# Optimization experiments

Measured on AMD Instinct MI355X. Metric: run time of the kernel, lower is better.

Reference implementation:

```python
import jax, jax.numpy as jnp
import numpy as np

L, N, E, H = 2048, 4, 1024, 16
DH = E // H


def setup_inputs() -> dict:
    key = jax.random.key(0)
    k1, k2, k3 = jax.random.split(key, 3)
    x = jax.random.normal(k1, (L, N, E), dtype=jnp.float32)
    # init like nn.Linear-ish scale to keep activations sane
    weight_qkv = jax.random.normal(k2, (3 * E, E), dtype=jnp.float32) * (E ** -0.5)
    weight_out = jax.random.normal(k3, (E, E), dtype=jnp.float32) * (E ** -0.5)
    return {"x": x, "weight_qkv": weight_qkv, "weight_out": weight_out}


def reference(x, weight_qkv, weight_out):
    # x: [L, N, E]; weight_qkv: [3E, E]; weight_out: [E, E]
    l, n, e = x.shape
    # fused QKV projection (F.linear: x @ W^T)
    qkv = jnp.einsum('lne,fe->lnf', x, weight_qkv)          # [L, N, 3E]
    qkv = qkv.reshape(l, n, 3, H, DH)
    q, k, v = jnp.moveaxis(qkv, 2, 0)                       # each [L, N, H, DH]
    q = jnp.transpose(q, (1, 2, 0, 3))                      # [N, H, L, DH]
    k = jnp.transpose(k, (1, 2, 0, 3))
    v = jnp.transpose(v, (1, 2, 0, 3))
    scale = DH ** -0.5
    scores = jnp.einsum('nhld,nhmd->nhlm', q, k) * scale    # [N, H, L, L]
    attn = jax.nn.softmax(scores, axis=-1)                  # dropout p=0.0 -> identity
    ctx = jnp.einsum('nhlm,nhmd->nhld', attn, v)            # [N, H, L, DH]
    ctx = jnp.transpose(ctx, (2, 0, 1, 3)).reshape(l, n, e) # [L, N, E]
    out = jnp.einsum('lne,fe->lnf', ctx, weight_out)        # output projection
    return out
```

## Files before the change

kernel.cpp:

```cpp
#include <hip/hip_runtime.h>
#include <hip/hip_bf16.h>

#define SEQ_L 2048
#define NBATCH 4
#define EDIM 1024
#define NHEAD 16
#define DHEAD 64

typedef __attribute__((ext_vector_type(4))) float f32x4;
typedef __attribute__((ext_vector_type(8))) short short8;
typedef unsigned short u16;
typedef unsigned long long u64;

#define QSCALE (0.125f * 1.44269504088896340736f)

__device__ __forceinline__ u16 f2bf(float f){
  unsigned u = __float_as_uint(f);
  u += 0x7fffu + ((u >> 16) & 1u);
  return (u16)(u >> 16);
}
__device__ __forceinline__ unsigned pack2bf(float a, float b){
  return ((unsigned)f2bf(b) << 16) | (unsigned)f2bf(a);
}
__device__ __forceinline__ u64 pack4bf(float a, float b, float c, float d){
  return ((u64)pack2bf(c, d) << 32) | (u64)pack2bf(a, b);
}
__device__ __forceinline__ float fexp2(float x){
  float r; asm("v_exp_f32 %0, %1" : "=v"(r) : "v"(x)); return r;
}

__global__ __launch_bounds__(256) void cvt_f32_bf16(const float* __restrict__ src,
                                                    u16* __restrict__ dst, int n4){
  int i = blockIdx.x * 256 + threadIdx.x;
  if (i < n4){
    float4 v = reinterpret_cast<const float4*>(src)[i];
    ushort4 o;
    o.x = f2bf(v.x); o.y = f2bf(v.y); o.z = f2bf(v.z); o.w = f2bf(v.w);
    reinterpret_cast<ushort4*>(dst)[i] = o;
  }
}

__global__ __launch_bounds__(256) void qkv_gemm(const u16* __restrict__ X,
                                                const u16* __restrict__ W,
                                                u16* __restrict__ Qd,
                                                u16* __restrict__ Kd,
                                                u16* __restrict__ Vt){
  __shared__ u16 SMEM[2*128*72];
  u16* XL = SMEM;
  u16* WL = SMEM + 128*72;
  const int tid = threadIdx.x;
  const int lane = tid & 63;
  const int wid = tid >> 6;
  const int wr = wid >> 1, wc = wid & 1;
  const int lr = lane & 15, lg = lane >> 4;
  const int bm = blockIdx.x, bn = blockIdx.y;
  f32x4 acc[4][4] = {};
  for (int kt = 0; kt < 16; ++kt){
    __syncthreads();
#pragma unroll
    for (int it = 0; it < 4; ++it){
      int c = tid + 256*it;
      int row = c >> 3, c8 = (c & 7) * 8;
      *(short8*)&XL[row*72 + c8] = *(const short8*)&X[(bm*128 + row)*EDIM + kt*64 + c8];
      *(short8*)&WL[row*72 + c8] = *(const short8*)&W[(bn*128 + row)*EDIM + kt*64 + c8];
    }
    __syncthreads();
#pragma unroll
    for (int ks = 0; ks < 2; ++ks){
      short8 a[4], b[4];
#pragma unroll
      for (int m = 0; m < 4; ++m)  a[m]  = *(short8*)&XL[(wr*64 + m*16  + lr)*72 + ks*32 + lg*8];
#pragma unroll
      for (int nn = 0; nn < 4; ++nn) b[nn] = *(short8*)&WL[(wc*64 + nn*16 + lr)*72 + ks*32 + lg*8];
#pragma unroll
      for (int m = 0; m < 4; ++m)
#pragma unroll
        for (int nn = 0; nn < 4; ++nn)
          acc[m][nn] = __builtin_amdgcn_mfma_f32_16x16x32_bf16(a[m], b[nn], acc[m][nn], 0, 0, 0);
    }
  }
  if (bn < 16){
#pragma unroll
    for (int m = 0; m < 4; ++m){
      const int i0 = bm*128 + wr*64 + m*16 + lg*4;
      const int l = i0 >> 2;
#pragma unroll
      for (int nn = 0; nn < 4; ++nn){
        const int f = bn*128 + wc*64 + nn*16 + lr;
        const int which = f >> 10;
        const int h = (f >> 6) & 15;
        const int d = f & 63;
        u16* dst = (which == 0) ? Qd : Kd;
        const float sc = (which == 0) ? QSCALE : 1.0f;
#pragma unroll
        for (int r = 0; r < 4; ++r)
          dst[((r*NHEAD + h)*SEQ_L + l)*DHEAD + d] = f2bf(acc[m][nn][r] * sc);
      }
    }
  } else {
    __syncthreads();
    u16* T = SMEM;
#pragma unroll
    for (int m = 0; m < 4; ++m){
      const int il0 = wr*64 + m*16 + lg*4;
#pragma unroll
      for (int nn = 0; nn < 4; ++nn){
        const int fl = wc*64 + nn*16 + lr;
        *(unsigned*)&T[fl*134 + il0]     = pack2bf(acc[m][nn][0], acc[m][nn][1]);
        *(unsigned*)&T[fl*134 + il0 + 2] = pack2bf(acc[m][nn][2], acc[m][nn][3]);
      }
    }
    __syncthreads();
    const int fl = tid & 127, nsel = tid >> 7;
    const int fV = bn*128 + fl - 2048;
    const int hh = fV >> 6, dd = fV & 63;
#pragma unroll
    for (int nn2 = 0; nn2 < 2; ++nn2){
      const int n = nsel*2 + nn2;
      u16 val[32];
#pragma unroll
      for (int ll = 0; ll < 32; ++ll)
        val[ll] = T[fl*134 + ll*4 + n];
      const size_t base = ((size_t)(n*NHEAD + hh)*DHEAD + dd)*SEQ_L + (size_t)bm*32;
#pragma unroll
      for (int j = 0; j < 4; ++j)
        *(short8*)&Vt[base + j*8] = *(short8*)&val[j*8];
    }
  }
}

__global__ __launch_bounds__(256) void attn(const u16* __restrict__ Qd,
                                            const u16* __restrict__ Kd,
                                            const u16* __restrict__ Vt,
                                            u16* __restrict__ Ctx){
  __shared__ u16 KL[64*72];
  __shared__ u16 VtL[64*72];
  __shared__ u16 PL[4*16*72];
  const int tid = threadIdx.x;
  const int lane = tid & 63;
  const int wid = tid >> 6;
  const int lr = lane & 15, lg = lane >> 4;
  const int head = blockIdx.y;
  const int n = head >> 4, h = head & 15;
  const u16* qh  = Qd + head * (SEQ_L * DHEAD);
  const u16* kh  = Kd + head * (SEQ_L * DHEAD);
  const u16* vth = Vt + (size_t)head * (DHEAD * SEQ_L);
  const int q0 = blockIdx.x * 64 + wid * 16;
  short8 bq[2];
#pragma unroll
  for (int ks = 0; ks < 2; ++ks)
    bq[ks] = *(const short8*)&qh[(q0 + lr)*DHEAD + ks*32 + lg*8];
  f32x4 acc[4] = {};
  float mrun = -1e30f, lrun = 0.0f;
  u16* myP = &PL[wid * 16 * 72];
  const int srow = tid >> 3, sc8 = (tid & 7) * 8;

  for (int kb0 = 0; kb0 < SEQ_L; kb0 += 64){
    __syncthreads();
    *(short8*)&KL[srow*72 + sc8]        = *(const short8*)&kh[(kb0 + srow)*DHEAD + sc8];
    *(short8*)&KL[(srow+32)*72 + sc8]   = *(const short8*)&kh[(kb0 + srow + 32)*DHEAD + sc8];
    *(short8*)&VtL[srow*72 + sc8]       = *(const short8*)&vth[(size_t)srow*SEQ_L + kb0 + sc8];
    *(short8*)&VtL[(srow+32)*72 + sc8]  = *(const short8*)&vth[(size_t)(srow+32)*SEQ_L + kb0 + sc8];
    __syncthreads();
    f32x4 s[4];
#pragma unroll
    for (int kb = 0; kb < 4; ++kb){
      short8 a0 = *(short8*)&KL[(kb*16 + lr)*72 + lg*8];
      short8 a1 = *(short8*)&KL[(kb*16 + lr)*72 + 32 + lg*8];
      f32x4 z = {0.f, 0.f, 0.f, 0.f};
      z = __builtin_amdgcn_mfma_f32_16x16x32_bf16(a0, bq[0], z, 0, 0, 0);
      z = __builtin_amdgcn_mfma_f32_16x16x32_bf16(a1, bq[1], z, 0, 0, 0);
      s[kb] = z;
    }
    float c0 = fmaxf(fmaxf(s[0][0], s[0][1]), fmaxf(s[0][2], s[0][3]));
    float c1 = fmaxf(fmaxf(s[1][0], s[1][1]), fmaxf(s[1][2], s[1][3]));
    float c2 = fmaxf(fmaxf(s[2][0], s[2][1]), fmaxf(s[2][2], s[2][3]));
    float c3 = fmaxf(fmaxf(s[3][0], s[3][1]), fmaxf(s[3][2], s[3][3]));
    float tmax = fmaxf(fmaxf(c0, c1), fmaxf(c2, c3));
    tmax = fmaxf(tmax, __shfl_xor(tmax, 16));
    tmax = fmaxf(tmax, __shfl_xor(tmax, 32));
    if (!__all(tmax <= mrun + 8.0f)){
      const float mnew = fmaxf(mrun, tmax);
      const float alpha = fexp2(mrun - mnew);
      lrun *= alpha;
      mrun = mnew;
      float ar[4];
#pragma unroll
      for (int r = 0; r < 4; ++r) ar[r] = __shfl(alpha, lg*4 + r);
#pragma unroll
      for (int db = 0; db < 4; ++db)
#pragma unroll
        for (int r = 0; r < 4; ++r) acc[db][r] *= ar[r];
    }
    float ps = 0.0f;
#pragma unroll
    for (int kb = 0; kb < 4; ++kb){
      const float p0 = fexp2(s[kb][0] - mrun);
      const float p1 = fexp2(s[kb][1] - mrun);
      const float p2 = fexp2(s[kb][2] - mrun);
      const float p3 = fexp2(s[kb][3] - mrun);
      *(u64*)&myP[lr*72 + kb*16 + lg*4] = pack4bf(p0, p1, p2, p3);
      ps += (p0 + p1) + (p2 + p3);
    }
    ps += __shfl_xor(ps, 16);
    ps += __shfl_xor(ps, 32);
    lrun += ps;
    asm volatile("s_waitcnt lgkmcnt(0)" ::: "memory");
    __builtin_amdgcn_sched_barrier(0);
#pragma unroll
    for (int c = 0; c < 2; ++c){
      short8 ap = *(short8*)&myP[lr*72 + c*32 + lg*8];
#pragma unroll
      for (int db = 0; db < 4; ++db){
        short8 bv = *(short8*)&VtL[(db*16 + lr)*72 + c*32 + lg*8];
        acc[db] = __builtin_amdgcn_mfma_f32_16x16x32_bf16(ap, bv, acc[db], 0, 0, 0);
      }
    }
  }
#pragma unroll
  for (int r = 0; r < 4; ++r){
    const float ld = __shfl(lrun, lg*4 + r);
    const float inv = 1.0f / ld;
    const int ql = q0 + lg*4 + r;
#pragma unroll
    for (int db = 0; db < 4; ++db)
      Ctx[(ql*NBATCH + n)*EDIM + h*DHEAD + db*16 + lr] = f2bf(acc[db][r] * inv);
  }
}

__global__ __launch_bounds__(256) void out_gemm(const u16* __restrict__ X,
                                                const u16* __restrict__ W,
                                                float* __restrict__ O){
  __shared__ u16 XL[128*72];
  __shared__ u16 WL[128*72];
  const int tid = threadIdx.x;
  const int lane = tid & 63;
  const int wid = tid >> 6;
  const int wr = wid >> 1, wc = wid & 1;
  const int lr = lane & 15, lg = lane >> 4;
  const int bm = blockIdx.x, bn = blockIdx.y;
  f32x4 acc[4][4] = {};
  for (int kt = 0; kt < 16; ++kt){
    __syncthreads();
#pragma unroll
    for (int it = 0; it < 4; ++it){
      int c = tid + 256*it;
      int row = c >> 3, c8 = (c & 7) * 8;
      *(short8*)&XL[row*72 + c8] = *(const short8*)&X[(bm*128 + row)*EDIM + kt*64 + c8];
      *(short8*)&WL[row*72 + c8] = *(const short8*)&W[(bn*128 + row)*EDIM + kt*64 + c8];
    }
    __syncthreads();
#pragma unroll
    for (int ks = 0; ks < 2; ++ks){
      short8 a[4], b[4];
#pragma unroll
      for (int m = 0; m < 4; ++m)  a[m]  = *(short8*)&XL[(wr*64 + m*16  + lr)*72 + ks*32 + lg*8];
#pragma unroll
      for (int nn = 0; nn < 4; ++nn) b[nn] = *(short8*)&WL[(wc*64 + nn*16 + lr)*72 + ks*32 + lg*8];
#pragma unroll
      for (int m = 0; m < 4; ++m)
#pragma unroll
        for (int nn = 0; nn < 4; ++nn)
          acc[m][nn] = __builtin_amdgcn_mfma_f32_16x16x32_bf16(a[m], b[nn], acc[m][nn], 0, 0, 0);
    }
  }
#pragma unroll
  for (int m = 0; m < 4; ++m){
    const int i0 = bm*128 + wr*64 + m*16 + lg*4;
#pragma unroll
    for (int nn = 0; nn < 4; ++nn){
      const int f = bn*128 + wc*64 + nn*16 + lr;
#pragma unroll
      for (int r = 0; r < 4; ++r)
        O[(size_t)(i0 + r)*EDIM + f] = acc[m][nn][r];
    }
  }
}

extern "C" void kernel_launch(void* const* d_in, const int* in_sizes, int n_in,
                              void* d_out, int out_size, void* d_ws, size_t ws_size,
                              hipStream_t stream){
  const float* x    = (const float*)d_in[0];
  const float* wqkv = (const float*)d_in[1];
  const float* wout = (const float*)d_in[2];
  float* out = (float*)d_out;
  u16* ws = (u16*)d_ws;
  const size_t XN  = (size_t)SEQ_L * NBATCH * EDIM;
  const size_t WQN = (size_t)3 * EDIM * EDIM;
  const size_t WON = (size_t)EDIM * EDIM;
  u16* xb    = ws;
  u16* wqkvb = xb + XN;
  u16* woutb = wqkvb + WQN;
  u16* qd    = woutb + WON;
  u16* kd    = qd + XN;
  u16* vt    = kd + XN;
  u16* ctx   = xb;

  cvt_f32_bf16<<<(int)(XN  / 1024), 256, 0, stream>>>(x,    xb,    (int)(XN  / 4));
  cvt_f32_bf16<<<(int)(WQN / 1024), 256, 0, stream>>>(wqkv, wqkvb, (int)(WQN / 4));
  cvt_f32_bf16<<<(int)(WON / 1024), 256, 0, stream>>>(wout, woutb, (int)(WON / 4));
  qkv_gemm<<<dim3(64, 24), 256, 0, stream>>>(xb, wqkvb, qd, kd, vt);
  attn    <<<dim3(32, 64), 256, 0, stream>>>(qd, kd, vt, ctx);
  out_gemm<<<dim3(64, 8),  256, 0, stream>>>(ctx, woutb, out);
}
```

Measured before the change: 269.1 us.

## Prefetch K/V tiles into registers, widen attention KV block to 128, use hardware bf16 pack

The attention kernel now processes 128 keys per iteration instead of 64, halving the number of block barriers and online-softmax rescale checks. It also prefetches the next K and V^T tile into registers while computing on the current tile in LDS, so global load latency overlaps with the MFMA work. Separately, the software round-to-nearest bf16 packing is replaced by the v_cvt_pk_bf16_f32 instruction in the conversion, QKV and attention kernels. The costs are higher register and LDS usage per block, which may lower occupancy.

After: 245.0 us. 9.0% less time.

```diff
diff --git a/kernel.cpp b/kernel.cpp
--- a/kernel.cpp
+++ b/kernel.cpp
@@ -19,11 +19,10 @@
   u += 0x7fffu + ((u >> 16) & 1u);
   return (u16)(u >> 16);
 }
-__device__ __forceinline__ unsigned pack2bf(float a, float b){
-  return ((unsigned)f2bf(b) << 16) | (unsigned)f2bf(a);
-}
-__device__ __forceinline__ u64 pack4bf(float a, float b, float c, float d){
-  return ((u64)pack2bf(c, d) << 32) | (u64)pack2bf(a, b);
+__device__ __forceinline__ unsigned cvt_pk_bf16(float a, float b){
+  unsigned r;
+  asm("v_cvt_pk_bf16_f32 %0, %1, %2" : "=v"(r) : "v"(a), "v"(b));
+  return r;
 }
 __device__ __forceinline__ float fexp2(float x){
   float r; asm("v_exp_f32 %0, %1" : "=v"(r) : "v"(x)); return r;
@@ -34,9 +33,10 @@
   int i = blockIdx.x * 256 + threadIdx.x;
   if (i < n4){
     float4 v = reinterpret_cast<const float4*>(src)[i];
-    ushort4 o;
-    o.x = f2bf(v.x); o.y = f2bf(v.y); o.z = f2bf(v.z); o.w = f2bf(v.w);
-    reinterpret_cast<ushort4*>(dst)[i] = o;
+    uint2 o;
+    o.x = cvt_pk_bf16(v.x, v.y);
+    o.y = cvt_pk_bf16(v.z, v.w);
+    *reinterpret_cast<uint2*>(dst + (size_t)i*4) = o;
   }
 }
 
@@ -106,8 +106,8 @@
 #pragma unroll
       for (int nn = 0; nn < 4; ++nn){
         const int fl = wc*64 + nn*16 + lr;
-        *(unsigned*)&T[fl*134 + il0]     = pack2bf(acc[m][nn][0], acc[m][nn][1]);
-        *(unsigned*)&T[fl*134 + il0 + 2] = pack2bf(acc[m][nn][2], acc[m][nn][3]);
+        *(unsigned*)&T[fl*134 + il0]     = cvt_pk_bf16(acc[m][nn][0], acc[m][nn][1]);
+        *(unsigned*)&T[fl*134 + il0 + 2] = cvt_pk_bf16(acc[m][nn][2], acc[m][nn][3]);
       }
     }
     __syncthreads();
@@ -133,9 +133,9 @@
                                             const u16* __restrict__ Kd,
                                             const u16* __restrict__ Vt,
                                             u16* __restrict__ Ctx){
-  __shared__ u16 KL[64*72];
-  __shared__ u16 VtL[64*72];
-  __shared__ u16 PL[4*16*72];
+  __shared__ u16 KL[128*72];
+  __shared__ u16 VtL[64*136];
+  __shared__ u16 PL[4*16*136];
   const int tid = threadIdx.x;
   const int lane = tid & 63;
   const int wid = tid >> 6;
@@ -152,19 +152,36 @@
     bq[ks] = *(const short8*)&qh[(q0 + lr)*DHEAD + ks*32 + lg*8];
   f32x4 acc[4] = {};
   float mrun = -1e30f, lrun = 0.0f;
-  u16* myP = &PL[wid * 16 * 72];
-  const int srow = tid >> 3, sc8 = (tid & 7) * 8;
-
-  for (int kb0 = 0; kb0 < SEQ_L; kb0 += 64){
-    __syncthreads();
-    *(short8*)&KL[srow*72 + sc8]        = *(const short8*)&kh[(kb0 + srow)*DHEAD + sc8];
-    *(short8*)&KL[(srow+32)*72 + sc8]   = *(const short8*)&kh[(kb0 + srow + 32)*DHEAD + sc8];
-    *(short8*)&VtL[srow*72 + sc8]       = *(const short8*)&vth[(size_t)srow*SEQ_L + kb0 + sc8];
-    *(short8*)&VtL[(srow+32)*72 + sc8]  = *(const short8*)&vth[(size_t)(srow+32)*SEQ_L + kb0 + sc8];
-    __syncthreads();
-    f32x4 s[4];
-#pragma unroll
-    for (int kb = 0; kb < 4; ++kb){
+  u16* myP = &PL[wid * 16 * 136];
+  const int kr = tid >> 3, kc8 = (tid & 7) * 8;
+  const int vr = tid >> 4, vc8 = (tid & 15) * 8;
+  short8 kreg[4], vreg[4];
+#pragma unroll
+  for (int j = 0; j < 4; ++j){
+    kreg[j] = *(const short8*)&kh[(j*32 + kr)*DHEAD + kc8];
+    vreg[j] = *(const short8*)&vth[(size_t)(j*16 + vr)*SEQ_L + vc8];
+  }
+
+  for (int t = 0; t < SEQ_L/128; ++t){
+    const int kb0 = t*128;
+    __syncthreads();
+#pragma unroll
+    for (int j = 0; j < 4; ++j){
+      *(short8*)&KL[(j*32 + kr)*72 + kc8]   = kreg[j];
+      *(short8*)&VtL[(j*16 + vr)*136 + vc8] = vreg[j];
+    }
+    __syncthreads();
+    if (t < SEQ_L/128 - 1){
+      const int kn = kb0 + 128;
+#pragma unroll
+      for (int j = 0; j < 4; ++j){
+        kreg[j] = *(const short8*)&kh[(kn + j*32 + kr)*DHEAD + kc8];
+        vreg[j] = *(const short8*)&vth[(size_t)(j*16 + vr)*SEQ_L + kn + vc8];
+      }
+    }
+    f32x4 s[8];
+#pragma unroll
+    for (int kb = 0; kb < 8; ++kb){
       short8 a0 = *(short8*)&KL[(kb*16 + lr)*72 + lg*8];
       short8 a1 = *(short8*)&KL[(kb*16 + lr)*72 + 32 + lg*8];
       f32x4 z = {0.f, 0.f, 0.f, 0.f};
@@ -172,11 +189,10 @@
       z = __builtin_amdgcn_mfma_f32_16x16x32_bf16(a1, bq[1], z, 0, 0, 0);
       s[kb] = z;
     }
-    float c0 = fmaxf(fmaxf(s[0][0], s[0][1]), fmaxf(s[0][2], s[0][3]));
-    float c1 = fmaxf(fmaxf(s[1][0], s[1][1]), fmaxf(s[1][2], s[1][3]));
-    float c2 = fmaxf(fmaxf(s[2][0], s[2][1]), fmaxf(s[2][2], s[2][3]));
-    float c3 = fmaxf(fmaxf(s[3][0], s[3][1]), fmaxf(s[3][2], s[3][3]));
-    float tmax = fmaxf(fmaxf(c0, c1), fmaxf(c2, c3));
+    float tmax = -1e30f;
+#pragma unroll
+    for (int kb = 0; kb < 8; ++kb)
+      tmax = fmaxf(tmax, fmaxf(fmaxf(s[kb][0], s[kb][1]), fmaxf(s[kb][2], s[kb][3])));
     tmax = fmaxf(tmax, __shfl_xor(tmax, 16));
     tmax = fmaxf(tmax, __shfl_xor(tmax, 32));
     if (!__all(tmax <= mrun + 8.0f)){
@@ -194,12 +210,14 @@
     }
     float ps = 0.0f;
 #pragma unroll
-    for (int kb = 0; kb < 4; ++kb){
+    for (int kb = 0; kb < 8; ++kb){
       const float p0 = fexp2(s[kb][0] - mrun);
       const float p1 = fexp2(s[kb][1] - mrun);
       const float p2 = fexp2(s[kb][2] - mrun);
       const float p3 = fexp2(s[kb][3] - mrun);
-      *(u64*)&myP[lr*72 + kb*16 + lg*4] = pack4bf(p0, p1, p2, p3);
+      const unsigned lo = cvt_pk_bf16(p0, p1);
+      const unsigned hi = cvt_pk_bf16(p2, p3);
+      *(u64*)&myP[lr*136 + kb*16 + lg*4] = ((u64)hi << 32) | (u64)lo;
       ps += (p0 + p1) + (p2 + p3);
     }
     ps += __shfl_xor(ps, 16);
@@ -208,11 +226,11 @@
     asm volatile("s_waitcnt lgkmcnt(0)" ::: "memory");
     __builtin_amdgcn_sched_barrier(0);
 #pragma unroll
-    for (int c = 0; c < 2; ++c){
-      short8 ap = *(short8*)&myP[lr*72 + c*32 + lg*8];
+    for (int c = 0; c < 4; ++c){
+      short8 ap = *(short8*)&myP[lr*136 + c*32 + lg*8];
 #pragma unroll
       for (int db = 0; db < 4; ++db){
-        short8 bv = *(short8*)&VtL[(db*16 + lr)*72 + c*32 + lg*8];
+        short8 bv = *(short8*)&VtL[(db*16 + lr)*136 + c*32 + lg*8];
         acc[db] = __builtin_amdgcn_mfma_f32_16x16x32_bf16(ap, bv, acc[db], 0, 0, 0);
       }
     }
```
